# Optimization experiments

Measured on AMD Instinct MI355X. Metric: run time of the kernel, lower is better.

Reference implementation:

```python
import jax, jax.numpy as jnp
import numpy as np

BATCH_SIZE = 4096          # B; representation has 2B rows
TEMPERATURE = 0.5


def setup_inputs() -> dict:
    key = jax.random.key(0)
    k1, k2, k3 = jax.random.split(key, 3)
    representation = jax.random.normal(k1, (2 * BATCH_SIZE, 128), dtype=jnp.float32)
    xrecon = jax.random.normal(k2, (2 * BATCH_SIZE, 512), dtype=jnp.float32)
    xorig = jax.random.normal(k3, (2 * BATCH_SIZE, 512), dtype=jnp.float32)
    return {"representation": representation, "xrecon": xrecon, "xorig": xorig}


def _xneg_loss(representation, batch_size, temperature):
    # Cosine similarity matrix [2B, 2B]
    n = representation / (jnp.linalg.norm(representation, axis=-1, keepdims=True) + 1e-8)
    sim = n @ n.T  # [2B, 2B]
    sim = sim / temperature
    two_b = 2 * batch_size
    # Positives: diag(sim, +B) then diag(sim, -B) -> [2B]
    l_pos = jnp.diagonal(sim, offset=batch_size)
    r_pos = jnp.diagonal(sim, offset=-batch_size)
    positives = jnp.concatenate([l_pos, r_pos])  # [2B]
    # NT-Xent: logits row i = [pos_i] + (row i minus diag and minus pos entry).
    # The union of {pos_i} and negatives_i is row i with only the main diagonal
    # removed, so CE with label 0 equals: -pos_i + logsumexp(row_i \ {diag}).
    neg_inf = jnp.finfo(sim.dtype).min
    eye = jnp.eye(two_b, dtype=bool)
    sim_no_diag = jnp.where(eye, neg_inf, sim)
    lse = jax.nn.logsumexp(sim_no_diag, axis=1)  # [2B]
    loss_sum = jnp.sum(lse - positives)           # CrossEntropyLoss(reduction='sum')
    return loss_sum / two_b


def reference(representation, xrecon, xorig):
    # reconstruction=True -> MSELoss (mean reduction)
    recon_loss = jnp.mean((xrecon - xorig) ** 2)
    loss = recon_loss
    # contrastive_loss=True
    closs = _xneg_loss(representation, BATCH_SIZE, TEMPERATURE)
    loss = loss + closs
    # distance_loss=True: MSE between the two halves of representation
    zi, zj = representation[:BATCH_SIZE], representation[BATCH_SIZE:]
    zrecon_loss = jnp.mean((zi - zj) ** 2)
    loss = loss + zrecon_loss
    return (loss, closs, recon_loss, zrecon_loss)
```

## Files before the change

### kernel.cpp

```cpp
#include <hip/hip_runtime.h>
#include <math.h>

#define BATCH 4096
#define NROWS (2 * BATCH)
#define D 128
#define DX 512

constexpr int NSPLIT = 16;
constexpr int NT = 4;
constexpr int SLOTS = NSPLIT * 2;

#define SCALE 1.698644f

#define WS_PART   0
#define WS_RECONP 262144
#define WS_ZRECP  (WS_RECONP + 1024)
#define WS_POSP   (WS_ZRECP + 256)
#define WS_LSEP   (WS_POSP + 256)
#define WS_NBF8   (WS_LSEP + 64)

typedef float f32x16 __attribute__((ext_vector_type(16)));
typedef long long i64;
typedef unsigned char u8;
typedef unsigned short u16;

__device__ __forceinline__ float wave_reduce(float v) {
    #pragma unroll
    for (int o = 32; o > 0; o >>= 1) v += __shfl_xor(v, o);
    return v;
}

__global__ __launch_bounds__(256) void k_prep(const float* __restrict__ rep,
                                              float* __restrict__ ws) {
    const int w = threadIdx.x >> 6, l = threadIdx.x & 63;
    const int wg = blockIdx.x * 4 + w;
    u8* nbf8 = (u8*)(ws + WS_NBF8);
    const int chunk = l >> 2, el = (l & 3) * 2;
    float zacc = 0.f, pacc = 0.f;
    #pragma unroll
    for (int p = 0; p < 4; ++p) {
        const int i = wg + p * 1024;
        float2 a = *reinterpret_cast<const float2*>(rep + i * D + l * 2);
        float2 b = *reinterpret_cast<const float2*>(rep + (i + BATCH) * D + l * 2);
        float dx = a.x - b.x, dy = a.y - b.y;
        float sa  = wave_reduce(a.x * a.x + a.y * a.y);
        float sb  = wave_reduce(b.x * b.x + b.y * b.y);
        float sab = wave_reduce(a.x * b.x + a.y * b.y);
        float sd  = wave_reduce(dx * dx + dy * dy);
        float ia = 1.0f / (sqrtf(sa) + 1e-8f);
        float ib = 1.0f / (sqrtf(sb) + 1e-8f);
        zacc += sd;
        pacc += sab * ia * ib;
        int pka = __builtin_amdgcn_cvt_pk_fp8_f32(a.x * ia * SCALE,
                                                  a.y * ia * SCALE, 0, false);
        int pkb = __builtin_amdgcn_cvt_pk_fp8_f32(b.x * ib * SCALE,
                                                  b.y * ib * SCALE, 0, false);
        *reinterpret_cast<u16*>(
            nbf8 + ((size_t)chunk * NROWS + i) * 8 + el) = (u16)pka;
        *reinterpret_cast<u16*>(
            nbf8 + ((size_t)chunk * NROWS + i + BATCH) * 8 + el) = (u16)pkb;
    }
    __shared__ float shz[4], shp[4];
    if (l == 0) { shz[w] = zacc; shp[w] = pacc; }
    __syncthreads();
    if (threadIdx.x == 0) {
        ws[WS_ZRECP + blockIdx.x] = shz[0] + shz[1] + shz[2] + shz[3];
        ws[WS_POSP + blockIdx.x] = 4.0f * (shp[0] + shp[1] + shp[2] + shp[3]);
    }
}

__global__ __launch_bounds__(256, 2) void k_lse(const float4* __restrict__ xr,
                                                const float4* __restrict__ xo,
                                                float* __restrict__ ws) {
    const u8* __restrict__ nbf8 = (const u8*)(ws + WS_NBF8);
    const int tid = threadIdx.x;
    const int w = tid >> 6, l = tid & 63;
    const int wr = w >> 1, wc = w & 1;
    const int rblk = blockIdx.x;
    const int split = blockIdx.y;
    const int R0 = rblk * 128;
    const int fid = rblk + 64 * split;

    i64 afrag[2][8];
    #pragma unroll
    for (int rb = 0; rb < 2; ++rb) {
        const int lr = R0 + wr * 64 + rb * 32 + (l & 31);
        #pragma unroll
        for (int s = 0; s < 8; ++s) {
            const int c = 2 * s + (l >> 5);
            afrag[rb][s] = *reinterpret_cast<const i64*>(
                nbf8 + ((size_t)c * NROWS + lr) * 8);
        }
    }

    int ridx = fid * 1024 + tid;
    float4 ra = xr[ridx], rbv = xo[ridx];

    float sumexp[2][16] = {};
    float racc = 0.f;

    for (int t = 0; t < NT; ++t) {
        const int C0 = split * (NT * 128) + t * 128;

        f32x16 acc[2][2] = {};
        #pragma unroll
        for (int s = 0; s < 8; ++s) {
            const int c = 2 * s + (l >> 5);
            const u8* base = nbf8 + (size_t)c * NROWS * 8;
            const int lc = C0 + wc * 64 + (l & 31);
            i64 b0 = *reinterpret_cast<const i64*>(base + (size_t)lc * 8);
            i64 b1 = *reinterpret_cast<const i64*>(base + (size_t)(lc + 32) * 8);
            acc[0][0] = __builtin_amdgcn_mfma_f32_32x32x16_fp8_fp8(
                afrag[0][s], b0, acc[0][0], 0, 0, 0);
            acc[0][1] = __builtin_amdgcn_mfma_f32_32x32x16_fp8_fp8(
                afrag[0][s], b1, acc[0][1], 0, 0, 0);
            acc[1][0] = __builtin_amdgcn_mfma_f32_32x32x16_fp8_fp8(
                afrag[1][s], b0, acc[1][0], 0, 0, 0);
            acc[1][1] = __builtin_amdgcn_mfma_f32_32x32x16_fp8_fp8(
                afrag[1][s], b1, acc[1][1], 0, 0, 0);
        }

        {
            float dx = ra.x - rbv.x, dy = ra.y - rbv.y;
            float dz = ra.z - rbv.z, dw2 = ra.w - rbv.w;
            racc += dx * dx + dy * dy + dz * dz + dw2 * dw2;
        }
        if (t + 1 < NT) {
            ridx = fid * 1024 + (t + 1) * 256 + tid;
            ra = xr[ridx];
            rbv = xo[ridx];
        }

        const bool diagt = ((C0 >> 7) * 0 == 0) && (C0 - R0 < 128) && (R0 - C0 < 128)
                           && (C0 == R0);
        #pragma unroll
        for (int rb = 0; rb < 2; ++rb) {
            #pragma unroll
            for (int cb = 0; cb < 2; ++cb) {
                const bool dmask = diagt && ((2 * wr + rb) == (2 * wc + cb));
                #pragma unroll
                for (int r = 0; r < 16; ++r) {
                    float e = __builtin_amdgcn_exp2f(acc[rb][cb][r]);
                    if (dmask) {
                        const int rrow = (r & 3) + 8 * (r >> 2) + 4 * (l >> 5);
                        if (rrow == (l & 31)) e = 0.0f;
                    }
                    sumexp[rb][r] += e;
                }
            }
        }
    }

    #pragma unroll
    for (int rb = 0; rb < 2; ++rb) {
        #pragma unroll
        for (int r = 0; r < 16; ++r) {
            float v = sumexp[rb][r];
            #pragma unroll
            for (int m = 1; m <= 16; m <<= 1) v += __shfl_xor(v, m);
            sumexp[rb][r] = v;
        }
    }
    if ((l & 31) == 0) {
        #pragma unroll
        for (int rb = 0; rb < 2; ++rb) {
            #pragma unroll
            for (int r = 0; r < 16; ++r) {
                const int row = R0 + wr * 64 + rb * 32
                              + (r & 3) + 8 * (r >> 2) + 4 * (l >> 5);
                ws[WS_PART + row * SLOTS + split * 2 + wc] = sumexp[rb][r];
            }
        }
    }

    racc = wave_reduce(racc);
    __shared__ float shr[4];
    if (l == 0) shr[w] = racc;
    __syncthreads();
    if (tid == 0) ws[WS_RECONP + fid] = shr[0] + shr[1] + shr[2] + shr[3];
}

__global__ __launch_bounds__(256) void k_rowlse(float* __restrict__ ws) {
    const int q = blockIdx.x, tid = threadIdx.x;
    const int j = tid & 127, h = tid >> 7;
    const int row = q * 128 + j;
    float s = 0.f;
    #pragma unroll
    for (int ss = 0; ss < SLOTS / 2; ++ss)
        s += ws[WS_PART + row * SLOTS + 2 * ss + h];
    __shared__ float red[128];
    if (h) red[j] = s;
    __syncthreads();
    float lg = 0.f;
    if (!h) lg = logf(s + red[j]);
    lg = wave_reduce(lg);
    __shared__ float sh[4];
    const int w = tid >> 6, l = tid & 63;
    if (l == 0) sh[w] = lg;
    __syncthreads();
    if (tid == 0) ws[WS_LSEP + q] = sh[0] + sh[1] + sh[2] + sh[3];
}

__global__ __launch_bounds__(256) void k_combine(const float* __restrict__ ws,
                                                 float* __restrict__ out) {
    const int tid = threadIdx.x;
    float lacc = (tid < 64) ? ws[WS_LSEP + tid] : 0.f;
    float racc = ws[WS_RECONP + tid] + ws[WS_RECONP + 256 + tid]
               + ws[WS_RECONP + 512 + tid] + ws[WS_RECONP + 768 + tid];
    float zacc = ws[WS_ZRECP + tid];
    float pacc = ws[WS_POSP + tid];

    lacc = wave_reduce(lacc);
    racc = wave_reduce(racc);
    zacc = wave_reduce(zacc);
    pacc = wave_reduce(pacc);

    __shared__ float sh[4][4];
    const int w = tid >> 6, l = tid & 63;
    if (l == 0) { sh[0][w] = lacc; sh[1][w] = racc; sh[2][w] = zacc; sh[3][w] = pacc; }
    __syncthreads();
    if (tid == 0) {
        float lse = sh[0][0] + sh[0][1] + sh[0][2] + sh[0][3];
        float rec = (sh[1][0] + sh[1][1] + sh[1][2] + sh[1][3]) / (float)(NROWS * DX);
        float zre = (sh[2][0] + sh[2][1] + sh[2][2] + sh[2][3]) / (float)(BATCH * D);
        float pos = sh[3][0] + sh[3][1] + sh[3][2] + sh[3][3];
        float closs = (lse - pos) / (float)NROWS;
        out[0] = rec + closs + zre;
        out[1] = closs;
        out[2] = rec;
        out[3] = zre;
    }
}

extern "C" void kernel_launch(void* const* d_in, const int* in_sizes, int n_in,
                              void* d_out, int out_size, void* d_ws, size_t ws_size,
                              hipStream_t stream) {
    const float* rep = (const float*)d_in[0];
    const float4* xr = (const float4*)d_in[1];
    const float4* xo = (const float4*)d_in[2];
    float* out = (float*)d_out;
    float* ws = (float*)d_ws;

    k_prep<<<256, 256, 0, stream>>>(rep, ws);
    dim3 grid(64, NSPLIT);
    k_lse<<<grid, 256, 0, stream>>>(xr, xo, ws);
    k_rowlse<<<64, 256, 0, stream>>>(ws);
    k_combine<<<1, 256, 0, stream>>>(ws, out);
}
```

Baseline: 37.50 us.

## Split LSE columns into 12 uneven groups and raise occupancy to 3 blocks/CU

Reduces the column split from 16 to 12, giving each block 5 or 6 column tiles via integer partitioning, so the grid drops to 768 blocks. The MFMA accumulator set is halved by processing one 32-column sub-block at a time, which lowers register pressure and allows a launch bound of 3 blocks per CU. The reconstruction MSE is redistributed as a grid-strided loop with a tail while-loop, and the workspace layout and combine step are resized to match. The aim is better latency hiding and a single-wave grid fit on the device, at the cost of uneven per-block work and reloading the B fragments per sub-block.

```diff
diff --git a/kernel.cpp b/kernel.cpp
--- a/kernel.cpp
+++ b/kernel.cpp
@@ -6,15 +6,17 @@
 #define D 128
 #define DX 512
 
-constexpr int NSPLIT = 16;
-constexpr int NT = 4;
+constexpr int NSPLIT = 12;
 constexpr int SLOTS = NSPLIT * 2;
+constexpr int NBLOCKS = 64 * NSPLIT;
+constexpr int TOT4 = NROWS * DX / 4;
+constexpr int RSTRIDE = NBLOCKS * 256;
 
 #define SCALE 1.698644f
 
 #define WS_PART   0
-#define WS_RECONP 262144
-#define WS_ZRECP  (WS_RECONP + 1024)
+#define WS_RECONP 196608
+#define WS_ZRECP  (WS_RECONP + 768)
 #define WS_POSP   (WS_ZRECP + 256)
 #define WS_LSEP   (WS_POSP + 256)
 #define WS_NBF8   (WS_LSEP + 64)
@@ -69,7 +71,7 @@
     }
 }
 
-__global__ __launch_bounds__(256, 2) void k_lse(const float4* __restrict__ xr,
+__global__ __launch_bounds__(256, 3) void k_lse(const float4* __restrict__ xr,
                                                 const float4* __restrict__ xo,
                                                 float* __restrict__ ws) {
     const u8* __restrict__ nbf8 = (const u8*)(ws + WS_NBF8);
@@ -79,6 +81,9 @@
     const int rblk = blockIdx.x;
     const int split = blockIdx.y;
     const int R0 = rblk * 128;
+    const int g0 = (split * 16) / 3;
+    const int g1 = ((split + 1) * 16) / 3;
+    const int nt = g1 - g0;
     const int fid = rblk + 64 * split;
 
     i64 afrag[2][8];
@@ -93,54 +98,38 @@
         }
     }
 
-    int ridx = fid * 1024 + tid;
+    int ridx = fid * 256 + tid;
+    bool rhave = true;
     float4 ra = xr[ridx], rbv = xo[ridx];
 
     float sumexp[2][16] = {};
     float racc = 0.f;
 
-    for (int t = 0; t < NT; ++t) {
-        const int C0 = split * (NT * 128) + t * 128;
-
-        f32x16 acc[2][2] = {};
-        #pragma unroll
-        for (int s = 0; s < 8; ++s) {
-            const int c = 2 * s + (l >> 5);
-            const u8* base = nbf8 + (size_t)c * NROWS * 8;
-            const int lc = C0 + wc * 64 + (l & 31);
-            i64 b0 = *reinterpret_cast<const i64*>(base + (size_t)lc * 8);
-            i64 b1 = *reinterpret_cast<const i64*>(base + (size_t)(lc + 32) * 8);
-            acc[0][0] = __builtin_amdgcn_mfma_f32_32x32x16_fp8_fp8(
-                afrag[0][s], b0, acc[0][0], 0, 0, 0);
-            acc[0][1] = __builtin_amdgcn_mfma_f32_32x32x16_fp8_fp8(
-                afrag[0][s], b1, acc[0][1], 0, 0, 0);
-            acc[1][0] = __builtin_amdgcn_mfma_f32_32x32x16_fp8_fp8(
-                afrag[1][s], b0, acc[1][0], 0, 0, 0);
-            acc[1][1] = __builtin_amdgcn_mfma_f32_32x32x16_fp8_fp8(
-                afrag[1][s], b1, acc[1][1], 0, 0, 0);
-        }
-
-        {
-            float dx = ra.x - rbv.x, dy = ra.y - rbv.y;
-            float dz = ra.z - rbv.z, dw2 = ra.w - rbv.w;
-            racc += dx * dx + dy * dy + dz * dz + dw2 * dw2;
-        }
-        if (t + 1 < NT) {
-            ridx = fid * 1024 + (t + 1) * 256 + tid;
-            ra = xr[ridx];
-            rbv = xo[ridx];
-        }
-
-        const bool diagt = ((C0 >> 7) * 0 == 0) && (C0 - R0 < 128) && (R0 - C0 < 128)
-                           && (C0 == R0);
-        #pragma unroll
-        for (int rb = 0; rb < 2; ++rb) {
-            #pragma unroll
-            for (int cb = 0; cb < 2; ++cb) {
+    for (int t = 0; t < nt; ++t) {
+        const int g = g0 + t;
+        const int C0 = g * 128;
+        const bool diagt = (g == rblk);
+
+        #pragma unroll
+        for (int cb = 0; cb < 2; ++cb) {
+            f32x16 acc[2] = {};
+            const int lc = C0 + wc * 64 + cb * 32 + (l & 31);
+            #pragma unroll
+            for (int s = 0; s < 8; ++s) {
+                const int c = 2 * s + (l >> 5);
+                i64 b = *reinterpret_cast<const i64*>(
+                    nbf8 + ((size_t)c * NROWS + lc) * 8);
+                acc[0] = __builtin_amdgcn_mfma_f32_32x32x16_fp8_fp8(
+                    afrag[0][s], b, acc[0], 0, 0, 0);
+                acc[1] = __builtin_amdgcn_mfma_f32_32x32x16_fp8_fp8(
+                    afrag[1][s], b, acc[1], 0, 0, 0);
+            }
+            #pragma unroll
+            for (int rb = 0; rb < 2; ++rb) {
                 const bool dmask = diagt && ((2 * wr + rb) == (2 * wc + cb));
                 #pragma unroll
                 for (int r = 0; r < 16; ++r) {
-                    float e = __builtin_amdgcn_exp2f(acc[rb][cb][r]);
+                    float e = __builtin_amdgcn_exp2f(acc[rb][r]);
                     if (dmask) {
                         const int rrow = (r & 3) + 8 * (r >> 2) + 4 * (l >> 5);
                         if (rrow == (l & 31)) e = 0.0f;
@@ -149,6 +138,23 @@
                 }
             }
         }
+
+        if (rhave) {
+            float dx = ra.x - rbv.x, dy = ra.y - rbv.y;
+            float dz = ra.z - rbv.z, dw2 = ra.w - rbv.w;
+            racc += dx * dx + dy * dy + dz * dz + dw2 * dw2;
+            ridx += RSTRIDE;
+            rhave = ridx < TOT4;
+            if (rhave) { ra = xr[ridx]; rbv = xo[ridx]; }
+        }
+    }
+    while (rhave) {
+        float dx = ra.x - rbv.x, dy = ra.y - rbv.y;
+        float dz = ra.z - rbv.z, dw2 = ra.w - rbv.w;
+        racc += dx * dx + dy * dy + dz * dz + dw2 * dw2;
+        ridx += RSTRIDE;
+        rhave = ridx < TOT4;
+        if (rhave) { ra = xr[ridx]; rbv = xo[ridx]; }
     }
 
     #pragma unroll
@@ -206,7 +212,7 @@
     const int tid = threadIdx.x;
     float lacc = (tid < 64) ? ws[WS_LSEP + tid] : 0.f;
     float racc = ws[WS_RECONP + tid] + ws[WS_RECONP + 256 + tid]
-               + ws[WS_RECONP + 512 + tid] + ws[WS_RECONP + 768 + tid];
+               + ws[WS_RECONP + 512 + tid];
     float zacc = ws[WS_ZRECP + tid];
     float pacc = ws[WS_POSP + tid];
 
```

Result: slower. 51.13 us (+36.3%).

## Halve column splits and double-buffer B fragment loads across tiles

Applied to the files above, without the earlier changes.

Cuts the column split count from 16 to 8 and doubles the tiles per block, so each block covers twice as many column tiles and there are half as many partial-sum slots. The tile loop is fully unrolled with ping-pong register buffers, so the next tile's B fragments and recon inputs are loaded while the current tile's MFMAs and exp work run. This is meant to hide global load latency and shrink the partial-sum traffic. In exchange it uses more registers, which may lower occupancy, and launches half as many blocks.

```diff
diff --git a/kernel.cpp b/kernel.cpp
--- a/kernel.cpp
+++ b/kernel.cpp
@@ -6,15 +6,15 @@
 #define D 128
 #define DX 512
 
-constexpr int NSPLIT = 16;
-constexpr int NT = 4;
+constexpr int NSPLIT = 8;
+constexpr int NT = 8;
 constexpr int SLOTS = NSPLIT * 2;
 
 #define SCALE 1.698644f
 
 #define WS_PART   0
-#define WS_RECONP 262144
-#define WS_ZRECP  (WS_RECONP + 1024)
+#define WS_RECONP 131072
+#define WS_ZRECP  (WS_RECONP + 512)
 #define WS_POSP   (WS_ZRECP + 256)
 #define WS_LSEP   (WS_POSP + 256)
 #define WS_NBF8   (WS_LSEP + 64)
@@ -93,46 +93,42 @@
         }
     }
 
-    int ridx = fid * 1024 + tid;
-    float4 ra = xr[ridx], rbv = xo[ridx];
-
+    i64 bufA[16], bufB[16];
+    float4 raA, rbA, raB, rbB;
     float sumexp[2][16] = {};
     float racc = 0.f;
 
-    for (int t = 0; t < NT; ++t) {
-        const int C0 = split * (NT * 128) + t * 128;
-
-        f32x16 acc[2][2] = {};
+    auto loadB = [&](i64 (&buf)[16], int t) {
+        const int lc = split * (NT * 128) + t * 128 + wc * 64 + (l & 31);
         #pragma unroll
         for (int s = 0; s < 8; ++s) {
             const int c = 2 * s + (l >> 5);
             const u8* base = nbf8 + (size_t)c * NROWS * 8;
-            const int lc = C0 + wc * 64 + (l & 31);
-            i64 b0 = *reinterpret_cast<const i64*>(base + (size_t)lc * 8);
-            i64 b1 = *reinterpret_cast<const i64*>(base + (size_t)(lc + 32) * 8);
+            buf[2 * s]     = *reinterpret_cast<const i64*>(base + (size_t)lc * 8);
+            buf[2 * s + 1] = *reinterpret_cast<const i64*>(base + (size_t)(lc + 32) * 8);
+        }
+    };
+
+    auto tile = [&](i64 (&buf)[16], int t, float4 ra, float4 rb2) {
+        const int C0 = split * (NT * 128) + t * 128;
+        const bool diagt = (C0 == R0);
+        f32x16 acc[2][2] = {};
+        #pragma unroll
+        for (int s = 0; s < 8; ++s) {
             acc[0][0] = __builtin_amdgcn_mfma_f32_32x32x16_fp8_fp8(
-                afrag[0][s], b0, acc[0][0], 0, 0, 0);
+                afrag[0][s], buf[2 * s], acc[0][0], 0, 0, 0);
             acc[0][1] = __builtin_amdgcn_mfma_f32_32x32x16_fp8_fp8(
-                afrag[0][s], b1, acc[0][1], 0, 0, 0);
+                afrag[0][s], buf[2 * s + 1], acc[0][1], 0, 0, 0);
             acc[1][0] = __builtin_amdgcn_mfma_f32_32x32x16_fp8_fp8(
-                afrag[1][s], b0, acc[1][0], 0, 0, 0);
+                afrag[1][s], buf[2 * s], acc[1][0], 0, 0, 0);
             acc[1][1] = __builtin_amdgcn_mfma_f32_32x32x16_fp8_fp8(
-                afrag[1][s], b1, acc[1][1], 0, 0, 0);
-        }
-
+                afrag[1][s], buf[2 * s + 1], acc[1][1], 0, 0, 0);
+        }
         {
-            float dx = ra.x - rbv.x, dy = ra.y - rbv.y;
-            float dz = ra.z - rbv.z, dw2 = ra.w - rbv.w;
+            float dx = ra.x - rb2.x, dy = ra.y - rb2.y;
+            float dz = ra.z - rb2.z, dw2 = ra.w - rb2.w;
             racc += dx * dx + dy * dy + dz * dz + dw2 * dw2;
         }
-        if (t + 1 < NT) {
-            ridx = fid * 1024 + (t + 1) * 256 + tid;
-            ra = xr[ridx];
-            rbv = xo[ridx];
-        }
-
-        const bool diagt = ((C0 >> 7) * 0 == 0) && (C0 - R0 < 128) && (R0 - C0 < 128)
-                           && (C0 == R0);
         #pragma unroll
         for (int rb = 0; rb < 2; ++rb) {
             #pragma unroll
@@ -149,6 +145,28 @@
                 }
             }
         }
+    };
+
+    loadB(bufA, 0);
+    {
+        const int ri = fid * 2048 + tid;
+        raA = xr[ri]; rbA = xo[ri];
+    }
+
+    #pragma unroll
+    for (int tt = 0; tt < NT; tt += 2) {
+        if (tt + 1 < NT) {
+            loadB(bufB, tt + 1);
+            const int ri = fid * 2048 + (tt + 1) * 256 + tid;
+            raB = xr[ri]; rbB = xo[ri];
+        }
+        tile(bufA, tt, raA, rbA);
+        if (tt + 2 < NT) {
+            loadB(bufA, tt + 2);
+            const int ri = fid * 2048 + (tt + 2) * 256 + tid;
+            raA = xr[ri]; rbA = xo[ri];
+        }
+        if (tt + 1 < NT) tile(bufB, tt + 1, raB, rbB);
     }
 
     #pragma unroll
@@ -205,8 +223,7 @@
                                                  float* __restrict__ out) {
     const int tid = threadIdx.x;
     float lacc = (tid < 64) ? ws[WS_LSEP + tid] : 0.f;
-    float racc = ws[WS_RECONP + tid] + ws[WS_RECONP + 256 + tid]
-               + ws[WS_RECONP + 512 + tid] + ws[WS_RECONP + 768 + tid];
+    float racc = ws[WS_RECONP + tid] + ws[WS_RECONP + 256 + tid];
     float zacc = ws[WS_ZRECP + tid];
     float pacc = ws[WS_POSP + tid];
 
```

Result: faster. 33.44 us, median of 2 (-10.8%).

## Exploit symmetry of similarity matrix to compute only upper-triangular tiles

Applied to the files above, without the earlier changes.

The LSE kernel now computes only half of the 64x64 block tiles of the symmetric cosine-similarity matrix, using a circulant assignment where each row block handles the next 32 column blocks. Each off-diagonal tile also produces column sums of exp, which are written to a new workspace region and added in k_rowlse. The intent is to roughly halve the MFMA and exp work. In exchange it adds extra cross-lane shuffles, stores and a longer reduction loop, and the last split is unbalanced because it carries an extra tile for half the row blocks. The B-fragment loads are also hoisted ahead of the MFMA loop.

```diff
diff --git a/kernel.cpp b/kernel.cpp
--- a/kernel.cpp
+++ b/kernel.cpp
@@ -6,15 +6,15 @@
 #define D 128
 #define DX 512
 
-constexpr int NSPLIT = 16;
-constexpr int NT = 4;
+constexpr int NSPLIT = 8;
 constexpr int SLOTS = NSPLIT * 2;
 
 #define SCALE 1.698644f
 
 #define WS_PART   0
-#define WS_RECONP 262144
-#define WS_ZRECP  (WS_RECONP + 1024)
+#define WS_CP     131072
+#define WS_RECONP 655360
+#define WS_ZRECP  (WS_RECONP + 512)
 #define WS_POSP   (WS_ZRECP + 256)
 #define WS_LSEP   (WS_POSP + 256)
 #define WS_NBF8   (WS_LSEP + 64)
@@ -77,67 +77,76 @@
     const int w = tid >> 6, l = tid & 63;
     const int wr = w >> 1, wc = w & 1;
     const int rblk = blockIdx.x;
-    const int split = blockIdx.y;
+    const int s = blockIdx.y;
     const int R0 = rblk * 128;
-    const int fid = rblk + 64 * split;
+    const int fid = rblk * 8 + s;
 
     i64 afrag[2][8];
     #pragma unroll
     for (int rb = 0; rb < 2; ++rb) {
         const int lr = R0 + wr * 64 + rb * 32 + (l & 31);
         #pragma unroll
-        for (int s = 0; s < 8; ++s) {
-            const int c = 2 * s + (l >> 5);
-            afrag[rb][s] = *reinterpret_cast<const i64*>(
+        for (int ss = 0; ss < 8; ++ss) {
+            const int c = 2 * ss + (l >> 5);
+            afrag[rb][ss] = *reinterpret_cast<const i64*>(
                 nbf8 + ((size_t)c * NROWS + lr) * 8);
         }
     }
-
-    int ridx = fid * 1024 + tid;
-    float4 ra = xr[ridx], rbv = xo[ridx];
 
     float sumexp[2][16] = {};
     float racc = 0.f;
 
-    for (int t = 0; t < NT; ++t) {
-        const int C0 = split * (NT * 128) + t * 128;
+    auto tile = [&](int j, int t) {
+        const int cblk = (rblk + j) & 63;
+        const int C0 = cblk * 128;
+
+        i64 buf[16];
+        const int lc = C0 + wc * 64 + (l & 31);
+        #pragma unroll
+        for (int ss = 0; ss < 8; ++ss) {
+            const int c = 2 * ss + (l >> 5);
+            const u8* base = nbf8 + (size_t)c * NROWS * 8;
+            buf[2 * ss]     = *reinterpret_cast<const i64*>(base + (size_t)lc * 8);
+            buf[2 * ss + 1] = *reinterpret_cast<const i64*>(base + (size_t)(lc + 32) * 8);
+        }
+
+        float4 ra0, rb0, ra1, rb1;
+        if (t >= 0) {
+            const int i0 = (fid * 8 + 2 * t) * 256 + tid;
+            const int i1 = (fid * 8 + 2 * t + 1) * 256 + tid;
+            ra0 = xr[i0]; rb0 = xo[i0];
+            ra1 = xr[i1]; rb1 = xo[i1];
+        }
 
         f32x16 acc[2][2] = {};
         #pragma unroll
-        for (int s = 0; s < 8; ++s) {
-            const int c = 2 * s + (l >> 5);
-            const u8* base = nbf8 + (size_t)c * NROWS * 8;
-            const int lc = C0 + wc * 64 + (l & 31);
-            i64 b0 = *reinterpret_cast<const i64*>(base + (size_t)lc * 8);
-            i64 b1 = *reinterpret_cast<const i64*>(base + (size_t)(lc + 32) * 8);
+        for (int ss = 0; ss < 8; ++ss) {
             acc[0][0] = __builtin_amdgcn_mfma_f32_32x32x16_fp8_fp8(
-                afrag[0][s], b0, acc[0][0], 0, 0, 0);
+                afrag[0][ss], buf[2 * ss], acc[0][0], 0, 0, 0);
             acc[0][1] = __builtin_amdgcn_mfma_f32_32x32x16_fp8_fp8(
-                afrag[0][s], b1, acc[0][1], 0, 0, 0);
+                afrag[0][ss], buf[2 * ss + 1], acc[0][1], 0, 0, 0);
             acc[1][0] = __builtin_amdgcn_mfma_f32_32x32x16_fp8_fp8(
-                afrag[1][s], b0, acc[1][0], 0, 0, 0);
+                afrag[1][ss], buf[2 * ss], acc[1][0], 0, 0, 0);
             acc[1][1] = __builtin_amdgcn_mfma_f32_32x32x16_fp8_fp8(
-                afrag[1][s], b1, acc[1][1], 0, 0, 0);
-        }
-
-        {
-            float dx = ra.x - rbv.x, dy = ra.y - rbv.y;
-            float dz = ra.z - rbv.z, dw2 = ra.w - rbv.w;
+                afrag[1][ss], buf[2 * ss + 1], acc[1][1], 0, 0, 0);
+        }
+
+        if (t >= 0) {
+            float dx = ra0.x - rb0.x, dy = ra0.y - rb0.y;
+            float dz = ra0.z - rb0.z, dw2 = ra0.w - rb0.w;
             racc += dx * dx + dy * dy + dz * dz + dw2 * dw2;
-        }
-        if (t + 1 < NT) {
-            ridx = fid * 1024 + (t + 1) * 256 + tid;
-            ra = xr[ridx];
-            rbv = xo[ridx];
-        }
-
-        const bool diagt = ((C0 >> 7) * 0 == 0) && (C0 - R0 < 128) && (R0 - C0 < 128)
-                           && (C0 == R0);
+            dx = ra1.x - rb1.x; dy = ra1.y - rb1.y;
+            dz = ra1.z - rb1.z; dw2 = ra1.w - rb1.w;
+            racc += dx * dx + dy * dy + dz * dz + dw2 * dw2;
+        }
+
+        const bool isdiag = (j == 0);
+        float colacc[2] = {0.f, 0.f};
         #pragma unroll
         for (int rb = 0; rb < 2; ++rb) {
             #pragma unroll
             for (int cb = 0; cb < 2; ++cb) {
-                const bool dmask = diagt && ((2 * wr + rb) == (2 * wc + cb));
+                const bool dmask = isdiag && ((2 * wr + rb) == (2 * wc + cb));
                 #pragma unroll
                 for (int r = 0; r < 16; ++r) {
                     float e = __builtin_amdgcn_exp2f(acc[rb][cb][r]);
@@ -146,9 +155,29 @@
                         if (rrow == (l & 31)) e = 0.0f;
                     }
                     sumexp[rb][r] += e;
+                    colacc[cb] += e;
                 }
             }
         }
+        if (!isdiag) {
+            #pragma unroll
+            for (int cb = 0; cb < 2; ++cb) {
+                float v = colacc[cb] + __shfl_xor(colacc[cb], 32);
+                if (l < 32) {
+                    const int col = wc * 64 + cb * 32 + l;
+                    ws[WS_CP + (((cblk * 32) + (j - 1)) * 2 + wr) * 128 + col] = v;
+                }
+            }
+        }
+    };
+
+    if (s < 7) {
+        const int jb = 4 * s + 1;
+        #pragma unroll
+        for (int t = 0; t < 4; ++t) tile(jb + t, t);
+    } else {
+        tile(29, 0); tile(30, 1); tile(31, 2); tile(0, 3);
+        if (rblk < 32) tile(32, -1);
     }
 
     #pragma unroll
@@ -168,7 +197,7 @@
             for (int r = 0; r < 16; ++r) {
                 const int row = R0 + wr * 64 + rb * 32
                               + (r & 3) + 8 * (r >> 2) + 4 * (l >> 5);
-                ws[WS_PART + row * SLOTS + split * 2 + wc] = sumexp[rb][r];
+                ws[WS_PART + row * SLOTS + s * 2 + wc] = sumexp[rb][r];
             }
         }
     }
@@ -182,17 +211,22 @@
 
 __global__ __launch_bounds__(256) void k_rowlse(float* __restrict__ ws) {
     const int q = blockIdx.x, tid = threadIdx.x;
-    const int j = tid & 127, h = tid >> 7;
-    const int row = q * 128 + j;
-    float s = 0.f;
+    const int col = tid & 127, h = tid >> 7;
+    const int row = q * 128 + col;
+    float ssum = 0.f;
     #pragma unroll
     for (int ss = 0; ss < SLOTS / 2; ++ss)
-        s += ws[WS_PART + row * SLOTS + 2 * ss + h];
+        ssum += ws[WS_PART + row * SLOTS + 2 * ss + h];
+    const float* cpq = ws + WS_CP + (size_t)q * 32 * 2 * 128;
+    for (int j = 1; j <= 31; ++j)
+        ssum += cpq[((j - 1) * 2 + h) * 128 + col];
+    if (q >= 32)
+        ssum += cpq[(31 * 2 + h) * 128 + col];
     __shared__ float red[128];
-    if (h) red[j] = s;
+    if (h) red[col] = ssum;
     __syncthreads();
     float lg = 0.f;
-    if (!h) lg = logf(s + red[j]);
+    if (!h) lg = logf(ssum + red[col]);
     lg = wave_reduce(lg);
     __shared__ float sh[4];
     const int w = tid >> 6, l = tid & 63;
@@ -205,8 +239,7 @@
                                                  float* __restrict__ out) {
     const int tid = threadIdx.x;
     float lacc = (tid < 64) ? ws[WS_LSEP + tid] : 0.f;
-    float racc = ws[WS_RECONP + tid] + ws[WS_RECONP + 256 + tid]
-               + ws[WS_RECONP + 512 + tid] + ws[WS_RECONP + 768 + tid];
+    float racc = ws[WS_RECONP + tid] + ws[WS_RECONP + 256 + tid];
     float zacc = ws[WS_ZRECP + tid];
     float pacc = ws[WS_POSP + tid];
 
```

Measured after the change: 48.50 us. +29.3%, slower.
